# Performance work log

Hardware: AMD Instinct MI355X
Metric: run time of the kernel (lower is better)

The kernel has to match this reference:

```python
import jax, jax.numpy as jnp
import numpy as np

DIM = 4096; H = 32; D = 128; EPS = 1e-5
BLOCK = 16
BD = 8; MAXB = 64                    # decode seqs, blocks per decode seq
PB = 2; PSEQ = 1024; TP = PB * PSEQ  # prefill: 2 seqs x 1024 tokens
TOK = TP + BD
NBLOCKS = BD * MAXB + TP // BLOCK    # 640
NEG = -1e30


def setup_inputs() -> dict:
    key = jax.random.key(0)
    ks = jax.random.split(key, 10)
    std = 0.02
    x = jax.random.normal(ks[0], (TOK, DIM), jnp.float32)
    key_heap = jax.random.normal(ks[1], (NBLOCKS, BLOCK, H, D), jnp.float32)
    val_heap = jax.random.normal(ks[2], (NBLOCKS, BLOCK, H, D), jnp.float32)
    # decode seq i owns blocks [i*MAXB, (i+1)*MAXB); context_len includes the new token
    ctx = jax.random.randint(ks[3], (BD,), 256, MAXB * BLOCK + 1).astype(jnp.int32)
    block_table = (jnp.arange(BD)[:, None] * MAXB + jnp.arange(MAXB)[None, :]).astype(jnp.int32)
    prefill_slots = BD * MAXB * BLOCK + jnp.arange(TP)      # prefill fills blocks after decode region
    decode_slots = jnp.arange(BD) * MAXB * BLOCK + (ctx - 1)  # newest-token slot per decode seq
    slot_mapping = jnp.concatenate([prefill_slots, decode_slots]).astype(jnp.int32)
    cu = (jnp.arange(PB + 1) * PSEQ).astype(jnp.int32)
    return dict(
        x=x, key_heap=key_heap, val_heap=val_heap,
        slot_mapping=slot_mapping, decode_block_table=block_table,
        decode_context_lens=ctx, prefill_cu_seqlens=cu,
        num_prefill_tokens=TP, prefill_max_seqlen=PSEQ, decode_max_seq_len=MAXB * BLOCK,
        norm1_w=1.0 + std * jax.random.normal(ks[4], (DIM,), jnp.float32),
        norm2_w=1.0 + std * jax.random.normal(ks[5], (DIM,), jnp.float32),
        w_qkv_w=std * jax.random.normal(ks[6], (3 * H * D, DIM), jnp.float32),
        wo_w=std * jax.random.normal(ks[7], (DIM, H * D), jnp.float32),
        w_gate_up_w=std * jax.random.normal(ks[8], (8 * DIM, DIM), jnp.float32),
        w2_w=std * jax.random.normal(ks[9], (DIM, 4 * DIM), jnp.float32),
    )


def _rmsnorm(x, w):
    return x * jax.lax.rsqrt(jnp.mean(x * x, -1, keepdims=True) + EPS) * w


def _forward(x, key_heap, val_heap, norm1_w, norm2_w, w_qkv_w, wo_w, w_gate_up_w, w2_w,
             slot_mapping, decode_block_table, decode_context_lens, prefill_cu_seqlens,
             num_prefill_tokens):
    T = x.shape[0]
    scale = 1.0 / np.sqrt(D)
    residual = x
    # fused norm1 -> QKV projection
    qkv = (_rmsnorm(x, norm1_w) @ w_qkv_w.T).reshape(T, 3, H, D)
    q, k, v = qkv[:, 0], qkv[:, 1], qkv[:, 2]
    # paged cache write (ops.reshape_and_cache)
    nb, bs = key_heap.shape[0], key_heap.shape[1]
    key_flat = key_heap.reshape(nb * bs, H, D).at[slot_mapping].set(k)
    val_flat = val_heap.reshape(nb * bs, H, D).at[slot_mapping].set(v)
    # prefill: varlen causal self-attention (flash_attn_varlen_func)
    Tp = num_prefill_tokens
    pos = jnp.arange(Tp)
    seg = jnp.searchsorted(prefill_cu_seqlens, pos, side='right') - 1
    mask = (seg[:, None] == seg[None, :]) & (pos[:, None] >= pos[None, :])  # [Tp,Tp]
    s = jnp.einsum('ihd,jhd->hij', q[:Tp], k[:Tp]) * scale
    attn_p = jnp.einsum('hij,jhd->ihd',
                        jax.nn.softmax(jnp.where(mask[None], s, NEG), -1), v[:Tp])
    # decode: paged attention over cached KV (ops.paged_attention_v2)
    kd = key_flat.reshape(nb, bs, H, D)[decode_block_table].reshape(BD, -1, H, D)
    vd = val_flat.reshape(nb, bs, H, D)[decode_block_table].reshape(BD, -1, H, D)
    L = kd.shape[1]
    sd = jnp.einsum('bhd,blhd->bhl', q[Tp:], kd) * scale
    dmask = jnp.arange(L)[None, :] < decode_context_lens[:, None]
    attn_d = jnp.einsum('bhl,blhd->bhd',
                        jax.nn.softmax(jnp.where(dmask[:, None, :], sd, NEG), -1), vd)
    attn = jnp.concatenate([attn_p.reshape(Tp, H * D), attn_d.reshape(BD, H * D)], 0)
    # MLP: wo + residual, norm2, SwiGLU, down-proj, residual
    h = attn @ wo_w.T + residual
    residual = h
    gu = _rmsnorm(h, norm2_w) @ w_gate_up_w.T
    g, u = jnp.split(gu, 2, -1)
    return (jax.nn.silu(g) * u) @ w2_w.T + residual


def reference(x, key_heap, val_heap, slot_mapping, decode_block_table, decode_context_lens,
              prefill_cu_seqlens, num_prefill_tokens, prefill_max_seqlen, decode_max_seq_len,
              norm1_w, norm2_w, w_qkv_w, wo_w, w_gate_up_w, w2_w):
    del prefill_max_seqlen, decode_max_seq_len  # kernel scheduling hints only
    return _forward(x, key_heap, val_heap, norm1_w, norm2_w, w_qkv_w, wo_w, w_gate_up_w, w2_w,
                    slot_mapping, decode_block_table, decode_context_lens, prefill_cu_seqlens,
                    num_prefill_tokens)
```

## Files before the change

### kernel.cpp

```cpp
#include <hip/hip_runtime.h>
#include <hip/hip_bf16.h>
#include <stdint.h>

#define DIMC   4096
#define HC     32
#define DC     128
#define TPC    2048
#define TOKC   2056
#define BDC    8
#define MAXBC  64
#define PSEQC  1024
#define QKVN   12288
#define FFNC   16384
#define PSCALE 0.08838834764831843f

typedef __attribute__((ext_vector_type(8))) short short8;
typedef __attribute__((ext_vector_type(4))) float f32x4;
typedef __attribute__((ext_vector_type(4))) unsigned short u16x4;
typedef __attribute__((ext_vector_type(8))) unsigned short u16x8;

__device__ inline unsigned short f2bf(float f) {
  union { float f; unsigned u; } v; v.f = f;
  unsigned r = v.u + 0x7FFFu + ((v.u >> 16) & 1u);
  return (unsigned short)(r >> 16);
}
__device__ inline float bf2f(unsigned short u) {
  union { unsigned u; float f; } v; v.u = ((unsigned)u) << 16;
  return v.f;
}
__device__ inline f32x4 mfma16(short8 a, short8 b, f32x4 c) {
  return __builtin_amdgcn_mfma_f32_16x16x32_bf16(a, b, c, 0, 0, 0);
}
__device__ inline void gload16(const void* g, void* l) {
  __builtin_amdgcn_global_load_lds(
      (const __attribute__((address_space(1))) void*)g,
      (__attribute__((address_space(3))) void*)l, 16, 0, 0);
}

__global__ __launch_bounds__(256) void cvt_w(
    const float* __restrict__ in, unsigned short* __restrict__ out, long n8)
{
  long i = (long)blockIdx.x * 256 + threadIdx.x;
  const long stride = (long)gridDim.x * 256;
  for (; i < n8; i += stride) {
    f32x4 a = ((const f32x4*)in)[2 * i];
    f32x4 b = ((const f32x4*)in)[2 * i + 1];
    u16x8 o;
#pragma unroll
    for (int j = 0; j < 4; ++j) { o[j] = f2bf(a[j]); o[j + 4] = f2bf(b[j]); }
    ((u16x8*)out)[i] = o;
  }
}

__global__ __launch_bounds__(256) void rmsnorm_k(
    const float* __restrict__ x, const float* __restrict__ w,
    unsigned short* __restrict__ out)
{
  const int row = blockIdx.x;
  const int tid = threadIdx.x;
  const f32x4* xr = (const f32x4*)(x + (size_t)row * DIMC);
  f32x4 v[4];
  float ss = 0.f;
#pragma unroll
  for (int i = 0; i < 4; ++i) {
    v[i] = xr[i * 256 + tid];
    ss += v[i][0]*v[i][0] + v[i][1]*v[i][1] + v[i][2]*v[i][2] + v[i][3]*v[i][3];
  }
  for (int off = 32; off; off >>= 1) ss += __shfl_xor(ss, off);
  __shared__ float sred[4];
  if ((tid & 63) == 0) sred[tid >> 6] = ss;
  __syncthreads();
  const float rms = rsqrtf((sred[0]+sred[1]+sred[2]+sred[3]) * (1.f/DIMC) + 1e-5f);
  const f32x4* wr = (const f32x4*)w;
#pragma unroll
  for (int i = 0; i < 4; ++i) {
    f32x4 wv = wr[i * 256 + tid];
    u16x4 o;
#pragma unroll
    for (int j = 0; j < 4; ++j) o[j] = f2bf(v[i][j] * rms * wv[j]);
    *(u16x4*)(out + (size_t)row * DIMC + (size_t)(i * 256 + tid) * 4) = o;
  }
}

template<int MODE, int BF16B>
__global__ __launch_bounds__(256) void gemm_bt(
    const unsigned short* __restrict__ A, const float* __restrict__ Bf,
    const unsigned short* __restrict__ Bh,
    float* __restrict__ Cf, unsigned short* __restrict__ Cb,
    const float* __restrict__ Res, int M, int N, int K)
{
  __shared__ unsigned short la[128 * 64];
  __shared__ unsigned short lb[128 * 64];
  const int tid = threadIdx.x;
  const int lane = tid & 63, wid = tid >> 6;
  const int wr = wid >> 1, wc = wid & 1;
  const int lhi = lane >> 4, llo = lane & 15;

  const int nM = (M + 127) >> 7;
  const int nwg = gridDim.x;
  const int orig = blockIdx.x;
  const int qq = nwg >> 3, rr = nwg & 7;
  const int xcd = orig & 7, lid = orig >> 3;
  const int wgid = (xcd < rr ? xcd * (qq + 1) : rr * (qq + 1) + (xcd - rr) * qq) + lid;
  const int bm = (wgid % nM) * 128;
  const int bn = (wgid / nM) * 128;

  const unsigned short* aSrc[4];
  const unsigned short* bSrcH[4];
  char* aDst[4];
  char* bDst[4];
#pragma unroll
  for (int p = 0; p < 4; ++p) {
    int slot = p * 256 + tid;
    int row = slot >> 3;
    int chunk = (slot & 7) ^ (row & 7);
    int gr = bm + row; gr = gr < M ? gr : M - 1;
    aSrc[p] = A + (size_t)gr * K + chunk * 8;
    aDst[p] = (char*)la + p * 4096 + wid * 1024;
    if (BF16B) {
      bSrcH[p] = Bh + (size_t)(bn + row) * K + chunk * 8;
      bDst[p] = (char*)lb + p * 4096 + wid * 1024;
    }
  }

  f32x4 acc[4][4] = {};

  for (int k0 = 0; k0 < K; k0 += 64) {
#pragma unroll
    for (int p = 0; p < 4; ++p) gload16(aSrc[p] + k0, aDst[p]);
    if (BF16B) {
#pragma unroll
      for (int p = 0; p < 4; ++p) gload16(bSrcH[p] + k0, bDst[p]);
    } else {
#pragma unroll
      for (int p = 0; p < 4; ++p) {
        int idx = p * 256 + tid;
        int row = idx >> 3, c8 = (idx & 7) << 3;
        const float* src = Bf + (size_t)(bn + row) * K + k0 + c8;
        f32x4 b0 = *(const f32x4*)src;
        f32x4 b1 = *(const f32x4*)(src + 4);
        short8 bv;
#pragma unroll
        for (int i = 0; i < 4; ++i) { bv[i] = (short)f2bf(b0[i]); bv[i+4] = (short)f2bf(b1[i]); }
        int byt = (row << 7) + (c8 << 1);
        byt ^= (row & 7) << 4;
        *(short8*)((char*)lb + byt) = bv;
      }
    }
    __syncthreads();
#pragma unroll
    for (int kk = 0; kk < 64; kk += 32) {
      short8 af[4], bfr[4];
#pragma unroll
      for (int m = 0; m < 4; ++m) {
        int row = wr * 64 + m * 16 + llo;
        int byt = (row << 7) + ((kk + lhi * 8) << 1);
        byt ^= (row & 7) << 4;
        af[m] = *(const short8*)((const char*)la + byt);
      }
#pragma unroll
      for (int n = 0; n < 4; ++n) {
        int row = wc * 64 + n * 16 + llo;
        int byt = (row << 7) + ((kk + lhi * 8) << 1);
        byt ^= (row & 7) << 4;
        bfr[n] = *(const short8*)((const char*)lb + byt);
      }
#pragma unroll
      for (int m = 0; m < 4; ++m)
#pragma unroll
        for (int n = 0; n < 4; ++n)
          acc[m][n] = mfma16(af[m], bfr[n], acc[m][n]);
    }
    __syncthreads();
  }

#pragma unroll
  for (int m = 0; m < 4; ++m) {
#pragma unroll
    for (int j = 0; j < 4; ++j) {
      int row = bm + wr * 64 + m * 16 + lhi * 4 + j;
      if (row < M) {
#pragma unroll
        for (int n = 0; n < 4; ++n) {
          int col = bn + wc * 64 + n * 16 + llo;
          float v = acc[m][n][j];
          if (MODE == 1) {
            v += Res[(size_t)row * N + col];
            Cf[(size_t)row * N + col] = v;
          } else {
            Cb[(size_t)row * N + col] = f2bf(v);
          }
        }
      }
    }
  }
}

__global__ __launch_bounds__(256) void prefill_attn(
    const unsigned short* __restrict__ qkv, unsigned short* __restrict__ attnb)
{
  const int h = blockIdx.x, qt = blockIdx.y, s = blockIdx.z;
  const int seq0 = s * PSEQC;
  const int q0 = qt * 64;
  const int tid = threadIdx.x;
  const int lane = tid & 63, w = tid >> 6;
  const int lhi = lane >> 4, llo = lane & 15;

  __shared__ unsigned short lk[64 * 128];
  __shared__ unsigned short lvt[128 * 72];
  __shared__ unsigned short lp[4][16 * 72];

  short8 qf[4];
  {
    const unsigned short* qrow =
        qkv + (size_t)(seq0 + q0 + w * 16 + llo) * QKVN + h * DC;
#pragma unroll
    for (int kk = 0; kk < 4; ++kk)
      qf[kk] = *(const short8*)(qrow + kk * 32 + lhi * 8);
  }

  float m_r[4], l_r[4];
#pragma unroll
  for (int r = 0; r < 4; ++r) { m_r[r] = -1e30f; l_r[r] = 0.f; }
  f32x4 oacc[8] = {};

  const int ntiles = qt + 1;
  for (int t = 0; t < ntiles; ++t) {
    const int j0 = t * 64;
#pragma unroll
    for (int p = 0; p < 4; ++p) {
      int idx = p * 256 + tid;
      int row = idx >> 4, c8 = (idx & 15) << 3;
      short8 kv = *(const short8*)(qkv + (size_t)(seq0 + j0 + row) * QKVN + DIMC + h * DC + c8);
      *(short8*)(lk + row * 128 + (c8 ^ ((row & 7) << 3))) = kv;
    }
#pragma unroll
    for (int p = 0; p < 4; ++p) {
      int idx = p * 256 + tid;
      int j = idx >> 4, c8 = (idx & 15) << 3;
      short8 vv = *(const short8*)(qkv + (size_t)(seq0 + j0 + j) * QKVN + 2 * DIMC + h * DC + c8);
#pragma unroll
      for (int i = 0; i < 8; ++i) {
        int d = c8 + i;
        int jj = j ^ (((d >> 3) & 7) << 3);
        lvt[d * 72 + jj] = (unsigned short)vv[i];
      }
    }
    __syncthreads();

    f32x4 sfr[4] = {};
#pragma unroll
    for (int n = 0; n < 4; ++n) {
      int row = n * 16 + llo;
#pragma unroll
      for (int kk = 0; kk < 4; ++kk) {
        int col = (kk * 32 + lhi * 8) ^ ((row & 7) << 3);
        short8 kf = *(const short8*)(lk + row * 128 + col);
        sfr[n] = mfma16(qf[kk], kf, sfr[n]);
      }
    }

    const bool diag = (t == ntiles - 1);
    const int qbase = q0 + w * 16 + lhi * 4;
    float pv[4][4];
#pragma unroll
    for (int r = 0; r < 4; ++r) {
      float mx = -1e30f;
#pragma unroll
      for (int n = 0; n < 4; ++n) {
        float sv = sfr[n][r] * PSCALE;
        if (diag && (j0 + n * 16 + llo > qbase + r)) sv = -1e30f;
        pv[n][r] = sv;
        mx = fmaxf(mx, sv);
      }
      for (int off = 8; off; off >>= 1) mx = fmaxf(mx, __shfl_xor(mx, off));
      float mnew = fmaxf(m_r[r], mx);
      float alpha = __expf(m_r[r] - mnew);
      m_r[r] = mnew;
      float rs = 0.f;
#pragma unroll
      for (int n = 0; n < 4; ++n) {
        float p = __expf(pv[n][r] - mnew);
        pv[n][r] = p;
        rs += p;
      }
      for (int off = 8; off; off >>= 1) rs += __shfl_xor(rs, off);
      l_r[r] = l_r[r] * alpha + rs;
#pragma unroll
      for (int f = 0; f < 8; ++f) oacc[f][r] *= alpha;
    }

    unsigned short* lpw = lp[w];
#pragma unroll
    for (int r = 0; r < 4; ++r)
#pragma unroll
      for (int n = 0; n < 4; ++n)
        lpw[(lhi * 4 + r) * 72 + n * 16 + llo] = f2bf(pv[n][r]);

#pragma unroll
    for (int kk = 0; kk < 2; ++kk) {
      short8 pf = *(const short8*)(lpw + llo * 72 + kk * 32 + lhi * 8);
#pragma unroll
      for (int f = 0; f < 8; ++f) {
        int d = f * 16 + llo;
        int jb = kk * 32 + lhi * 8;
        int jj = jb ^ (((d >> 3) & 7) << 3);
        short8 vf = *(const short8*)(lvt + d * 72 + jj);
        oacc[f] = mfma16(pf, vf, oacc[f]);
      }
    }
    __syncthreads();
  }

#pragma unroll
  for (int r = 0; r < 4; ++r) {
    int row = seq0 + q0 + w * 16 + lhi * 4 + r;
    float inv = 1.f / l_r[r];
#pragma unroll
    for (int f = 0; f < 8; ++f)
      attnb[(size_t)row * DIMC + h * DC + f * 16 + llo] = f2bf(oacc[f][r] * inv);
  }
}

__global__ __launch_bounds__(256) void decode_attn(
    const unsigned short* __restrict__ qkv,
    const float* __restrict__ kheap, const float* __restrict__ vheap,
    const int* __restrict__ btab, const int* __restrict__ ctxl,
    unsigned short* __restrict__ attnb)
{
  const int h = blockIdx.x, b = blockIdx.y;
  const int ctx = ctxl[b];
  const int tq = TPC + b;
  const int tid = threadIdx.x;
  __shared__ float sq[DC];
  __shared__ float sp[1024];
  __shared__ float sred[4];
  __shared__ float obuf[DC];

  const unsigned short* qrow = qkv + (size_t)tq * QKVN + h * DC;
  if (tid < DC) sq[tid] = bf2f(qrow[tid]);
  __syncthreads();

  float lmax = -1e30f;
#pragma unroll
  for (int i = 0; i < 4; ++i) {
    int l = i * 256 + tid;
    float sv = -1e30f;
    if (l < ctx) {
      float accd = 0.f;
      if (l == ctx - 1) {
        const unsigned short* kn = qkv + (size_t)tq * QKVN + DIMC + h * DC;
        for (int d = 0; d < DC; ++d) accd += sq[d] * bf2f(kn[d]);
      } else {
        int blk = btab[b * MAXBC + (l >> 4)];
        const float* kp = kheap + (((size_t)blk * 16 + (l & 15)) * HC + h) * DC;
#pragma unroll
        for (int d = 0; d < DC; d += 4) {
          f32x4 kv = *(const f32x4*)(kp + d);
          accd += sq[d] * kv[0] + sq[d+1] * kv[1] + sq[d+2] * kv[2] + sq[d+3] * kv[3];
        }
      }
      sv = accd * PSCALE;
    }
    sp[l] = sv;
    lmax = fmaxf(lmax, sv);
  }
  for (int off = 32; off; off >>= 1) lmax = fmaxf(lmax, __shfl_xor(lmax, off));
  if ((tid & 63) == 0) sred[tid >> 6] = lmax;
  __syncthreads();
  const float m = fmaxf(fmaxf(sred[0], sred[1]), fmaxf(sred[2], sred[3]));
  __syncthreads();

  float lsum = 0.f;
#pragma unroll
  for (int i = 0; i < 4; ++i) {
    int l = i * 256 + tid;
    float p = __expf(sp[l] - m);
    sp[l] = p;
    lsum += p;
  }
  for (int off = 32; off; off >>= 1) lsum += __shfl_xor(lsum, off);
  if ((tid & 63) == 0) sred[tid >> 6] = lsum;
  __syncthreads();
  const float denom = sred[0] + sred[1] + sred[2] + sred[3];

  const int d = tid & 127, half = tid >> 7;
  float o = 0.f;
  for (int l = half; l < ctx; l += 2) {
    float p = sp[l];
    float v;
    if (l == ctx - 1) {
      v = bf2f(qkv[(size_t)tq * QKVN + 2 * DIMC + h * DC + d]);
    } else {
      int blk = btab[b * MAXBC + (l >> 4)];
      v = vheap[(((size_t)blk * 16 + (l & 15)) * HC + h) * DC + d];
    }
    o += p * v;
  }
  if (half) obuf[d] = o;
  __syncthreads();
  if (!half)
    attnb[(size_t)tq * DIMC + h * DC + d] = f2bf((o + obuf[d]) / denom);
}

__global__ __launch_bounds__(256) void silu_mul(
    const unsigned short* __restrict__ gu, unsigned short* __restrict__ act)
{
  size_t chunk = (size_t)blockIdx.x * 256 + threadIdx.x;
  size_t row = chunk >> 11;
  int c = (int)(chunk & 2047) << 3;
  const unsigned short* g = gu + row * (2 * FFNC) + c;
  u16x8 gv = *(const u16x8*)g;
  u16x8 uv = *(const u16x8*)(g + FFNC);
  u16x8 o;
#pragma unroll
  for (int i = 0; i < 8; ++i) {
    float gf = bf2f(gv[i]);
    float uf = bf2f(uv[i]);
    float sf = gf / (1.f + __expf(-gf));
    o[i] = f2bf(sf * uf);
  }
  *(u16x8*)(act + row * FFNC + c) = o;
}

extern "C" void kernel_launch(void* const* d_in, const int* in_sizes, int n_in,
                              void* d_out, int out_size, void* d_ws, size_t ws_size,
                              hipStream_t stream) {
  const float* x     = (const float*)d_in[0];
  const float* kheap = (const float*)d_in[1];
  const float* vheap = (const float*)d_in[2];
  const int*   btab  = (const int*)d_in[4];
  const int*   ctxl  = (const int*)d_in[5];
  const float* n1w   = (const float*)d_in[10];
  const float* n2w   = (const float*)d_in[11];
  const float* wqkv  = (const float*)d_in[12];
  const float* wo    = (const float*)d_in[13];
  const float* wgu   = (const float*)d_in[14];
  const float* w2    = (const float*)d_in[15];
  float* out = (float*)d_out;

  char* ws = (char*)d_ws;
  unsigned short* xn   = (unsigned short*)(ws);
  unsigned short* qkvb = (unsigned short*)(ws + 16842752);
  unsigned short* actb = qkvb;
  unsigned short* attn = (unsigned short*)(ws + 16842752 + 67371008);
  float*          hbuf = (float*)(ws + 16842752 + 67371008 + 16842752);
  unsigned short* gub  = (unsigned short*)(ws + 16842752 + 67371008 + 16842752 + 33685504);

  const size_t wbase = 269484032;
  const bool bw = ws_size >= wbase + 536870912ull;
  unsigned short* wqkv_h = (unsigned short*)(ws + wbase);
  unsigned short* wo_h   = (unsigned short*)(ws + wbase + 100663296);
  unsigned short* wgu_h  = (unsigned short*)(ws + wbase + 100663296 + 33554432);
  unsigned short* w2_h   = (unsigned short*)(ws + wbase + 100663296 + 33554432 + 268435456);

  if (bw) {
    cvt_w<<<2048, 256, 0, stream>>>(wqkv, wqkv_h, (long)QKVN * DIMC / 8);
    cvt_w<<<2048, 256, 0, stream>>>(wo,   wo_h,   (long)DIMC * DIMC / 8);
    cvt_w<<<2048, 256, 0, stream>>>(wgu,  wgu_h,  (long)2 * FFNC * DIMC / 8);
    cvt_w<<<2048, 256, 0, stream>>>(w2,   w2_h,   (long)DIMC * FFNC / 8);
  }

  const int nM = 17;

  rmsnorm_k<<<TOKC, 256, 0, stream>>>(x, n1w, xn);
  if (bw) gemm_bt<2,1><<<nM * (QKVN/128), 256, 0, stream>>>(xn, nullptr, wqkv_h, nullptr, qkvb, nullptr, TOKC, QKVN, DIMC);
  else    gemm_bt<2,0><<<nM * (QKVN/128), 256, 0, stream>>>(xn, wqkv, nullptr, nullptr, qkvb, nullptr, TOKC, QKVN, DIMC);
  prefill_attn<<<dim3(HC, PSEQC / 64, 2), 256, 0, stream>>>(qkvb, attn);
  decode_attn<<<dim3(HC, BDC), 256, 0, stream>>>(qkvb, kheap, vheap, btab, ctxl, attn);
  if (bw) gemm_bt<1,1><<<nM * (DIMC/128), 256, 0, stream>>>(attn, nullptr, wo_h, hbuf, nullptr, x, TOKC, DIMC, DIMC);
  else    gemm_bt<1,0><<<nM * (DIMC/128), 256, 0, stream>>>(attn, wo, nullptr, hbuf, nullptr, x, TOKC, DIMC, DIMC);
  rmsnorm_k<<<TOKC, 256, 0, stream>>>(hbuf, n2w, xn);
  if (bw) gemm_bt<2,1><<<nM * (2*FFNC/128), 256, 0, stream>>>(xn, nullptr, wgu_h, nullptr, gub, nullptr, TOKC, 2*FFNC, DIMC);
  else    gemm_bt<2,0><<<nM * (2*FFNC/128), 256, 0, stream>>>(xn, wgu, nullptr, nullptr, gub, nullptr, TOKC, 2*FFNC, DIMC);
  silu_mul<<<(TOKC * (FFNC / 8)) / 256, 256, 0, stream>>>(gub, actb);
  if (bw) gemm_bt<1,1><<<nM * (DIMC/128), 256, 0, stream>>>(actb, nullptr, w2_h, out, nullptr, hbuf, TOKC, DIMC, FFNC);
  else    gemm_bt<1,0><<<nM * (DIMC/128), 256, 0, stream>>>(actb, w2, nullptr, out, nullptr, hbuf, TOKC, DIMC, FFNC);
}
```

Measured before the change: 2.163 ms.

## Add 256x256 8-wave ping-pong GEMM kernel for QKV, gate-up and down projections

Adds a new bf16 GEMM kernel with 256x256 output tiles, 512 threads per block and a double-buffered 128KB LDS layout. It splits each K step into four quadrant sub-GEMMs, interleaving global-to-LDS staging with MFMA work under explicit waitcnt, barriers and setprio. It also remaps block IDs across the 8 XCDs so neighbouring tiles share L2. The QKV, gate-up and down-projection GEMMs use it when bf16 weights are available; the wo GEMM keeps the old kernel. The larger tiles raise operand reuse and cut global traffic, at the cost of fewer blocks (9 row tiles with padding waste, since 2056 rows exceeds 8x256) and heavy LDS use per block.

Result: faster. 2.017 ms (-6.7%).

```diff
diff --git a/kernel.cpp b/kernel.cpp
--- a/kernel.cpp
+++ b/kernel.cpp
@@ -80,6 +80,134 @@
     for (int j = 0; j < 4; ++j) o[j] = f2bf(v[i][j] * rms * wv[j]);
     *(u16x4*)(out + (size_t)row * DIMC + (size_t)(i * 256 + tid) * 4) = o;
   }
+}
+
+template<int MODE>
+__global__ __launch_bounds__(512, 2) void gemm8p(
+    const unsigned short* __restrict__ A, const unsigned short* __restrict__ Bh,
+    float* __restrict__ Cf, unsigned short* __restrict__ Cb,
+    const float* __restrict__ Res, int M, int N, int K)
+{
+  __shared__ char ldsc[131072];
+  const int tid = threadIdx.x;
+  const int lane = tid & 63, wid = tid >> 6;
+  const int wr = wid >> 2, wc = wid & 3;
+  const int lhi = lane >> 4, llo = lane & 15;
+
+  const int nM = (M + 255) >> 8;
+  const int nwg = gridDim.x, orig = blockIdx.x;
+  const int qq = nwg >> 3, rr = nwg & 7;
+  const int xcd = orig & 7, lid = orig >> 3;
+  const int wgid = (xcd < rr ? xcd*(qq+1) : rr*(qq+1) + (xcd-rr)*qq) + lid;
+  const int bm = (wgid % nM) << 8;
+  const int bn = (wgid / nM) << 8;
+
+  const unsigned short* src[2][2][2];
+#pragma unroll
+  for (int i = 0; i < 2; ++i) {
+    int s = i * 512 + tid;
+    int row = s >> 3;
+    int chunk = (s & 7) ^ (row & 7);
+#pragma unroll
+    for (int h = 0; h < 2; ++h) {
+      int ga = bm + h * 128 + row; ga = ga < M ? ga : M - 1;
+      src[0][h][i] = A  + (size_t)ga * K + chunk * 8;
+      src[1][h][i] = Bh + (size_t)(bn + h * 128 + row) * K + chunk * 8;
+    }
+  }
+  const int NT = K >> 6;
+
+#define STG(U, OP, H) do { \
+    int bb_ = (((U) & 1) << 16) + ((OP) << 15) + ((H) << 14) + (wid << 10); \
+    gload16(src[OP][H][0] + ((size_t)(U) << 6), ldsc + bb_); \
+    gload16(src[OP][H][1] + ((size_t)(U) << 6), ldsc + bb_ + 8192); \
+  } while (0)
+
+#define LDA(PB, HA) do { _Pragma("unroll") for (int m_ = 0; m_ < 4; ++m_) { \
+    int row_ = wr*64 + m_*16 + llo; \
+    int rb_ = (PB) + ((HA) << 14) + row_*128; int sx_ = (row_ & 7) << 4; \
+    ar[m_][0] = *(const short8*)(ldsc + rb_ + ((lhi*16) ^ sx_)); \
+    ar[m_][1] = *(const short8*)(ldsc + rb_ + ((64 + lhi*16) ^ sx_)); } } while (0)
+
+#define LDB(PB, HB, DST) do { _Pragma("unroll") for (int n_ = 0; n_ < 2; ++n_) { \
+    int row_ = wc*32 + n_*16 + llo; \
+    int rb_ = (PB) + 32768 + ((HB) << 14) + row_*128; int sx_ = (row_ & 7) << 4; \
+    DST[n_][0] = *(const short8*)(ldsc + rb_ + ((lhi*16) ^ sx_)); \
+    DST[n_][1] = *(const short8*)(ldsc + rb_ + ((64 + lhi*16) ^ sx_)); } } while (0)
+
+#define MM(QA, QB, B_) do { __builtin_amdgcn_s_setprio(1); \
+    _Pragma("unroll") for (int m_ = 0; m_ < 4; ++m_) \
+    _Pragma("unroll") for (int n_ = 0; n_ < 2; ++n_) { \
+      acc[QA][QB][m_][n_] = mfma16(ar[m_][0], B_[n_][0], acc[QA][QB][m_][n_]); \
+      acc[QA][QB][m_][n_] = mfma16(ar[m_][1], B_[n_][1], acc[QA][QB][m_][n_]); } \
+    __builtin_amdgcn_s_setprio(0); } while (0)
+
+#define WAITL do { asm volatile("s_waitcnt lgkmcnt(0)" ::: "memory"); \
+    __builtin_amdgcn_sched_barrier(0); } while (0)
+#define BAR __builtin_amdgcn_s_barrier()
+
+  f32x4 acc[2][2][4][2] = {};
+  short8 ar[4][2], b0[2][2], b1[2][2];
+
+  STG(0, 0, 0); STG(0, 0, 1); STG(0, 1, 0); STG(0, 1, 1);
+  STG(1, 0, 0); STG(1, 1, 0); STG(1, 1, 1);
+  asm volatile("s_waitcnt vmcnt(6)" ::: "memory");
+  BAR;
+
+  for (int t = 0; t < NT; ++t) {
+    const int pb = (t & 1) << 16;
+    LDA(pb, 0); LDB(pb, 0, b0);
+    if (t + 1 < NT) STG(t + 1, 0, 1);
+    BAR; WAITL;
+    MM(0, 0, b0);
+    BAR;
+    LDB(pb, 1, b1);
+    if (t + 2 < NT) STG(t + 2, 0, 0);
+    BAR; WAITL;
+    MM(0, 1, b1);
+    BAR;
+    LDA(pb, 1);
+    if (t + 2 < NT) STG(t + 2, 1, 0);
+    BAR; WAITL;
+    MM(1, 1, b1);
+    BAR;
+    if (t + 2 < NT) {
+      STG(t + 2, 1, 1);
+      asm volatile("s_waitcnt vmcnt(6)" ::: "memory");
+    } else {
+      asm volatile("s_waitcnt vmcnt(0)" ::: "memory");
+    }
+    BAR;
+    __builtin_amdgcn_sched_barrier(0);
+    MM(1, 0, b0);
+    BAR;
+  }
+
+#pragma unroll
+  for (int qa = 0; qa < 2; ++qa)
+#pragma unroll
+  for (int m_ = 0; m_ < 4; ++m_)
+#pragma unroll
+  for (int j = 0; j < 4; ++j) {
+    int row = bm + qa*128 + wr*64 + m_*16 + lhi*4 + j;
+    if (row < M) {
+#pragma unroll
+      for (int qb = 0; qb < 2; ++qb)
+#pragma unroll
+      for (int n_ = 0; n_ < 2; ++n_) {
+        int col = bn + qb*128 + wc*32 + n_*16 + llo;
+        float v = acc[qa][qb][m_][n_][j];
+        if (MODE == 1) { v += Res[(size_t)row*N + col]; Cf[(size_t)row*N + col] = v; }
+        else Cb[(size_t)row*N + col] = f2bf(v);
+      }
+    }
+  }
+#undef STG
+#undef LDA
+#undef LDB
+#undef MM
+#undef WAITL
+#undef BAR
 }
 
 template<int MODE, int BF16B>
@@ -136,12 +264,12 @@
       for (int p = 0; p < 4; ++p) {
         int idx = p * 256 + tid;
         int row = idx >> 3, c8 = (idx & 7) << 3;
-        const float* src = Bf + (size_t)(bn + row) * K + k0 + c8;
-        f32x4 b0 = *(const f32x4*)src;
-        f32x4 b1 = *(const f32x4*)(src + 4);
+        const float* srcf = Bf + (size_t)(bn + row) * K + k0 + c8;
+        f32x4 v0 = *(const f32x4*)srcf;
+        f32x4 v1 = *(const f32x4*)(srcf + 4);
         short8 bv;
 #pragma unroll
-        for (int i = 0; i < 4; ++i) { bv[i] = (short)f2bf(b0[i]); bv[i+4] = (short)f2bf(b1[i]); }
+        for (int i = 0; i < 4; ++i) { bv[i] = (short)f2bf(v0[i]); bv[i+4] = (short)f2bf(v1[i]); }
         int byt = (row << 7) + (c8 << 1);
         byt ^= (row & 7) << 4;
         *(short8*)((char*)lb + byt) = bv;
@@ -461,19 +589,20 @@
     cvt_w<<<2048, 256, 0, stream>>>(w2,   w2_h,   (long)DIMC * FFNC / 8);
   }
 
-  const int nM = 17;
+  const int nM8 = 9;
+  const int nM4 = 17;
 
   rmsnorm_k<<<TOKC, 256, 0, stream>>>(x, n1w, xn);
-  if (bw) gemm_bt<2,1><<<nM * (QKVN/128), 256, 0, stream>>>(xn, nullptr, wqkv_h, nullptr, qkvb, nullptr, TOKC, QKVN, DIMC);
-  else    gemm_bt<2,0><<<nM * (QKVN/128), 256, 0, stream>>>(xn, wqkv, nullptr, nullptr, qkvb, nullptr, TOKC, QKVN, DIMC);
+  if (bw) gemm8p<2><<<nM8 * (QKVN/256), 512, 0, stream>>>(xn, wqkv_h, nullptr, qkvb, nullptr, TOKC, QKVN, DIMC);
+  else    gemm_bt<2,0><<<nM4 * (QKVN/128), 256, 0, stream>>>(xn, wqkv, nullptr, nullptr, qkvb, nullptr, TOKC, QKVN, DIMC);
   prefill_attn<<<dim3(HC, PSEQC / 64, 2), 256, 0, stream>>>(qkvb, attn);
   decode_attn<<<dim3(HC, BDC), 256, 0, stream>>>(qkvb, kheap, vheap, btab, ctxl, attn);
-  if (bw) gemm_bt<1,1><<<nM * (DIMC/128), 256, 0, stream>>>(attn, nullptr, wo_h, hbuf, nullptr, x, TOKC, DIMC, DIMC);
-  else    gemm_bt<1,0><<<nM * (DIMC/128), 256, 0, stream>>>(attn, wo, nullptr, hbuf, nullptr, x, TOKC, DIMC, DIMC);
+  if (bw) gemm_bt<1,1><<<nM4 * (DIMC/128), 256, 0, stream>>>(attn, nullptr, wo_h, hbuf, nullptr, x, TOKC, DIMC, DIMC);
+  else    gemm_bt<1,0><<<nM4 * (DIMC/128), 256, 0, stream>>>(attn, wo, nullptr, hbuf, nullptr, x, TOKC, DIMC, DIMC);
   rmsnorm_k<<<TOKC, 256, 0, stream>>>(hbuf, n2w, xn);
-  if (bw) gemm_bt<2,1><<<nM * (2*FFNC/128), 256, 0, stream>>>(xn, nullptr, wgu_h, nullptr, gub, nullptr, TOKC, 2*FFNC, DIMC);
-  else    gemm_bt<2,0><<<nM * (2*FFNC/128), 256, 0, stream>>>(xn, wgu, nullptr, nullptr, gub, nullptr, TOKC, 2*FFNC, DIMC);
+  if (bw) gemm8p<2><<<nM8 * (2*FFNC/256), 512, 0, stream>>>(xn, wgu_h, nullptr, gub, nullptr, TOKC, 2*FFNC, DIMC);
+  else    gemm_bt<2,0><<<nM4 * (2*FFNC/128), 256, 0, stream>>>(xn, wgu, nullptr, nullptr, gub, nullptr, TOKC, 2*FFNC, DIMC);
   silu_mul<<<(TOKC * (FFNC / 8)) / 256, 256, 0, stream>>>(gub, actb);
-  if (bw) gemm_bt<1,1><<<nM * (DIMC/128), 256, 0, stream>>>(actb, nullptr, w2_h, out, nullptr, hbuf, TOKC, DIMC, FFNC);
-  else    gemm_bt<1,0><<<nM * (DIMC/128), 256, 0, stream>>>(actb, w2, nullptr, out, nullptr, hbuf, TOKC, DIMC, FFNC);
-}
+  if (bw) gemm8p<1><<<nM8 * (DIMC/256), 512, 0, stream>>>(actb, w2_h, out, nullptr, hbuf, TOKC, DIMC, FFNC);
+  else    gemm_bt<1,0><<<nM4 * (DIMC/128), 256, 0, stream>>>(actb, w2, nullptr, out, nullptr, hbuf, TOKC, DIMC, FFNC);
+}
```
